# Kernel tuning notes

Hardware: AMD Instinct MI355X
Metric: run time of the kernel (lower is better)

Reference implementation:

```python
import jax, jax.numpy as jnp
import numpy as np

SIGMA = 1.0  # init kwarg sigma

def _rbf_kernel(A):
    # K[i,j] = exp(-0.5 * ||a_i - a_j||^2 / sigma^2)
    sq = jnp.sum(A * A, axis=1)                      # [n]
    d2 = sq[:, None] + sq[None, :] - 2.0 * (A @ A.T)  # [n, n]
    return jnp.exp(-0.5 * d2 / (SIGMA ** 2))

def _double_center(K):
    # C K C with C = I - 11^T/n, done in O(n^2) via mean subtraction
    row = K.mean(axis=1, keepdims=True)
    col = K.mean(axis=0, keepdims=True)
    tot = K.mean()
    return K - row - col + tot

def setup_inputs() -> dict:
    key = jax.random.key(0)
    kx, ky = jax.random.split(key)
    X = jax.random.normal(kx, (4096, 512), dtype=jnp.float32)
    Y = jax.random.normal(ky, (4096, 512), dtype=jnp.float32)
    return {"X": X, "Y": Y}

def reference(X, Y):
    n = X.shape[0]
    KXc = _double_center(_rbf_kernel(X))
    KYc = _double_center(_rbf_kernel(Y))
    # trace(KX C KY C) = sum(center(KX) * center(KY)) since K symmetric, C idempotent
    hsic = jnp.sum(KXc * KYc) / ((n - 1) ** 2)
    return hsic
```

## Files before the change

kernel.cpp:

```cpp
#include <hip/hip_runtime.h>
#include <hip/hip_bf16.h>

namespace {

constexpr int N = 4096;
constexpr int D = 512;
constexpr int BM = 64;
constexpr int BK = 64;
constexpr int KITERS = D / BK;
constexpr int NB = N / BM;
constexpr int NBLK = NB * (NB + 1) / 2;
constexpr int TILEB = BM * BK;
constexpr int PANELB = BM * D;

constexpr size_t OFF_XB  = 0;
constexpr size_t OFF_YB  = (size_t)N * D;
constexpr size_t OFF_SQX = OFF_YB + (size_t)N * D;
constexpr size_t OFF_SQY = OFF_SQX + (size_t)N * 4;
constexpr size_t OFF_SX  = OFF_SQY + (size_t)N * 4;
constexpr size_t OFF_SY  = OFF_SX + (size_t)N * 4;
constexpr size_t OFF_T1  = OFF_SY + (size_t)N * 4;
constexpr size_t WS_NEED = OFF_T1 + 4;

constexpr float D2_SKIP = 240.f;

typedef __attribute__((ext_vector_type(4))) float floatx4;
typedef __attribute__((ext_vector_type(2))) long longx2;

__device__ inline unsigned short bf16bits(float f) {
  return __builtin_bit_cast(unsigned short, __float2bfloat16(f));
}

__global__ void prep_kernel(const float* __restrict__ X, const float* __restrict__ Y,
                            unsigned char* __restrict__ Xf8, unsigned char* __restrict__ Yf8,
                            float* __restrict__ sqX, float* __restrict__ sqY,
                            float* __restrict__ sX, float* __restrict__ sY,
                            float* __restrict__ T1) {
  const int wave = threadIdx.x >> 6, lane = threadIdx.x & 63;
  const int row = blockIdx.x * 4 + wave;
  const int m = blockIdx.y;
  const float* __restrict__ src = m ? Y : X;
  unsigned char* __restrict__ dst = m ? Yf8 : Xf8;
  float* __restrict__ dsq = m ? sqY : sqX;

  if (threadIdx.x < 4) {
    float* z = m ? sY : sX;
    z[blockIdx.x * 4 + threadIdx.x] = 0.f;
  }
  if (blockIdx.x == 0 && m == 0 && threadIdx.x == 0) *T1 = 0.f;

  const float4* s4 = (const float4*)(src + (size_t)row * D);
  float4 v0 = s4[lane * 2];
  float4 v1 = s4[lane * 2 + 1];
  float acc = v0.x * v0.x + v0.y * v0.y + v0.z * v0.z + v0.w * v0.w
            + v1.x * v1.x + v1.y * v1.y + v1.z * v1.z + v1.w * v1.w;

  unsigned int w0 = 0, w1 = 0;
  w0 = __builtin_amdgcn_cvt_pk_fp8_f32(v0.x, v0.y, w0, false);
  w0 = __builtin_amdgcn_cvt_pk_fp8_f32(v0.z, v0.w, w0, true);
  w1 = __builtin_amdgcn_cvt_pk_fp8_f32(v1.x, v1.y, w1, false);
  w1 = __builtin_amdgcn_cvt_pk_fp8_f32(v1.z, v1.w, w1, true);
  const unsigned long long pk =
      (unsigned long long)w0 | ((unsigned long long)w1 << 32);

  const int p    = row >> 6;
  const int nib  = (row >> 4) & 3;
  const int cl   = row & 15;
  const int ks   = lane >> 3;
  const int pass = (lane >> 2) & 1;
  const int quad = lane & 3;
  const size_t off = (size_t)p * PANELB + (size_t)ks * TILEB +
                     nib * 1024 + quad * 256 + cl * 16 + pass * 8;
  *(unsigned long long*)(dst + off) = pk;

#pragma unroll
  for (int mm = 32; mm >= 1; mm >>= 1) acc += __shfl_xor(acc, mm, 64);
  if (lane == 0) dsq[row] = acc;
}

__launch_bounds__(256, 4)
__global__ void hsic_main(const unsigned char* __restrict__ Xf8,
                          const unsigned char* __restrict__ Yf8,
                          const float* __restrict__ sqX, const float* __restrict__ sqY,
                          float* __restrict__ sX, float* __restrict__ sY,
                          float* __restrict__ T1) {
  const int b = blockIdx.x;
  int idx = (b & 7) * (NBLK / 8) + (b >> 3);

  const float nf = (float)NB + 0.5f;
  int bI = (int)(nf - sqrtf(nf * nf - 2.0f * (float)idx));
  if (bI < 0) bI = 0;
  if (bI >= NB) bI = NB - 1;
  while (bI * NB - bI * (bI - 1) / 2 > idx) --bI;
  while ((bI + 1) * NB - (bI + 1) * bI / 2 <= idx) ++bI;
  const int bJ = bI + (idx - (bI * NB - bI * (bI - 1) / 2));
  const bool offdiag = (bI != bJ);

  const int tid = threadIdx.x;
  const int lane = tid & 63, wave = tid >> 6;
  const int wm = wave >> 1, wn = wave & 1;
  const int quad = lane >> 4, cl = lane & 15;
  const int lane16 = lane << 4;

  const unsigned char* gAx = Xf8 + (size_t)bI * PANELB + wm * 2048 + lane16;
  const unsigned char* gBx = Xf8 + (size_t)bJ * PANELB + wn * 2048 + lane16;
  const unsigned char* gAy = Yf8 + (size_t)bI * PANELB + wm * 2048 + lane16;
  const unsigned char* gBy = Yf8 + (size_t)bJ * PANELB + wn * 2048 + lane16;

  floatx4 acc[2][2];
#pragma unroll
  for (int i = 0; i < 2; ++i)
#pragma unroll
    for (int j = 0; j < 2; ++j) acc[i][j] = (floatx4){0.f, 0.f, 0.f, 0.f};

  const int Ib = bI * BM + wm * 32;
  const int Jb = bJ * BM + wn * 32;

  unsigned int kxp[2][2][2];
  unsigned int fmask = 0;
  float t1l = 0.f;

#pragma unroll
  for (int ks = 0; ks < KITERS; ++ks) {
    longx2 af[2], bf[2];
#pragma unroll
    for (int mi = 0; mi < 2; ++mi)
      af[mi] = *(const longx2*)(gAx + (size_t)ks * TILEB + mi * 1024);
#pragma unroll
    for (int ni = 0; ni < 2; ++ni)
      bf[ni] = *(const longx2*)(gBx + (size_t)ks * TILEB + ni * 1024);
#pragma unroll
    for (int mi = 0; mi < 2; ++mi)
#pragma unroll
      for (int ni = 0; ni < 2; ++ni) {
        acc[mi][ni] = __builtin_amdgcn_mfma_f32_16x16x32_fp8_fp8(af[mi][0], bf[ni][0], acc[mi][ni], 0, 0, 0);
        acc[mi][ni] = __builtin_amdgcn_mfma_f32_16x16x32_fp8_fp8(af[mi][1], bf[ni][1], acc[mi][ni], 0, 0, 0);
      }
  }

  {
    float rx[2][4];
    float cx[2];
#pragma unroll
    for (int mi = 0; mi < 2; ++mi)
#pragma unroll
      for (int r = 0; r < 4; ++r) rx[mi][r] = 0.f;
#pragma unroll
    for (int ni = 0; ni < 2; ++ni) cx[ni] = 0.f;

#pragma unroll
    for (int mi = 0; mi < 2; ++mi) {
      const int ig0 = Ib + mi * 16 + quad * 4;
      float sxi[4];
#pragma unroll
      for (int r = 0; r < 4; ++r) sxi[r] = sqX[ig0 + r];
#pragma unroll
      for (int ni = 0; ni < 2; ++ni) {
        const int jg = Jb + ni * 16 + cl;
        const float sxj = sqX[jg];
        float d2x[4];
        bool lflag = false;
#pragma unroll
        for (int r = 0; r < 4; ++r) {
          const int ig = ig0 + r;
          d2x[r] = sxi[r] + sxj - 2.f * acc[mi][ni][r];
          lflag |= (d2x[r] < D2_SKIP) | (ig == jg);
        }
        float kxv[4] = {0.f, 0.f, 0.f, 0.f};
        if (__any(lflag)) {
          fmask |= (1u << (mi * 2 + ni));
#pragma unroll
          for (int r = 0; r < 4; ++r) {
            const int ig = ig0 + r;
            kxv[r] = (ig == jg) ? 1.f : __expf(-0.5f * d2x[r]);
            rx[mi][r] += kxv[r];
            cx[ni] += kxv[r];
          }
        }
        kxp[mi][ni][0] = (unsigned)bf16bits(kxv[0]) | ((unsigned)bf16bits(kxv[1]) << 16);
        kxp[mi][ni][1] = (unsigned)bf16bits(kxv[2]) | ((unsigned)bf16bits(kxv[3]) << 16);
        acc[mi][ni] = (floatx4){0.f, 0.f, 0.f, 0.f};
      }
    }

    if (fmask != 0) {
#pragma unroll
      for (int mi = 0; mi < 2; ++mi)
#pragma unroll
        for (int r = 0; r < 4; ++r) {
          float vx = rx[mi][r];
#pragma unroll
          for (int mm = 1; mm < 16; mm <<= 1) vx += __shfl_xor(vx, mm, 16);
          rx[mi][r] = vx;
        }
      if (cl == 0) {
#pragma unroll
        for (int mi = 0; mi < 2; ++mi)
#pragma unroll
          for (int r = 0; r < 4; ++r)
            atomicAdd(&sX[Ib + mi * 16 + quad * 4 + r], rx[mi][r]);
      }
      if (offdiag) {
#pragma unroll
        for (int ni = 0; ni < 2; ++ni) {
          float vx = cx[ni];
          vx += __shfl_xor(vx, 16, 64);
          vx += __shfl_xor(vx, 32, 64);
          if (quad == 0) atomicAdd(&sX[Jb + ni * 16 + cl], vx);
        }
      }
    }
  }

#pragma unroll
  for (int ks = 0; ks < KITERS; ++ks) {
    longx2 af[2], bf[2];
#pragma unroll
    for (int mi = 0; mi < 2; ++mi)
      af[mi] = *(const longx2*)(gAy + (size_t)ks * TILEB + mi * 1024);
#pragma unroll
    for (int ni = 0; ni < 2; ++ni)
      bf[ni] = *(const longx2*)(gBy + (size_t)ks * TILEB + ni * 1024);
#pragma unroll
    for (int mi = 0; mi < 2; ++mi)
#pragma unroll
      for (int ni = 0; ni < 2; ++ni) {
        acc[mi][ni] = __builtin_amdgcn_mfma_f32_16x16x32_fp8_fp8(af[mi][0], bf[ni][0], acc[mi][ni], 0, 0, 0);
        acc[mi][ni] = __builtin_amdgcn_mfma_f32_16x16x32_fp8_fp8(af[mi][1], bf[ni][1], acc[mi][ni], 0, 0, 0);
      }
  }

  {
    float ry[2][4];
    float cy[2];
    bool anyy = false;
#pragma unroll
    for (int mi = 0; mi < 2; ++mi)
#pragma unroll
      for (int r = 0; r < 4; ++r) ry[mi][r] = 0.f;
#pragma unroll
    for (int ni = 0; ni < 2; ++ni) cy[ni] = 0.f;

#pragma unroll
    for (int mi = 0; mi < 2; ++mi) {
      const int ig0 = Ib + mi * 16 + quad * 4;
      float syi[4];
#pragma unroll
      for (int r = 0; r < 4; ++r) syi[r] = sqY[ig0 + r];
#pragma unroll
      for (int ni = 0; ni < 2; ++ni) {
        const int jg = Jb + ni * 16 + cl;
        const float syj = sqY[jg];
        float d2y[4];
        bool lflag = false;
#pragma unroll
        for (int r = 0; r < 4; ++r) {
          const int ig = ig0 + r;
          d2y[r] = syi[r] + syj - 2.f * acc[mi][ni][r];
          lflag |= (d2y[r] < D2_SKIP) | (ig == jg);
        }
        const bool xb = (fmask >> (mi * 2 + ni)) & 1u;
        if (__any(lflag) || xb) {
          anyy = true;
          float kyv[4];
#pragma unroll
          for (int r = 0; r < 4; ++r) {
            const int ig = ig0 + r;
            kyv[r] = (ig == jg) ? 1.f : __expf(-0.5f * d2y[r]);
            ry[mi][r] += kyv[r];
            cy[ni] += kyv[r];
          }
          if (xb) {
            const float kx0 = __builtin_bit_cast(float, (kxp[mi][ni][0] & 0xFFFFu) << 16);
            const float kx1 = __builtin_bit_cast(float, kxp[mi][ni][0] & 0xFFFF0000u);
            const float kx2 = __builtin_bit_cast(float, (kxp[mi][ni][1] & 0xFFFFu) << 16);
            const float kx3 = __builtin_bit_cast(float, kxp[mi][ni][1] & 0xFFFF0000u);
            t1l += kx0 * kyv[0] + kx1 * kyv[1] + kx2 * kyv[2] + kx3 * kyv[3];
          }
        }
      }
    }

    if (anyy) {
#pragma unroll
      for (int mi = 0; mi < 2; ++mi)
#pragma unroll
        for (int r = 0; r < 4; ++r) {
          float vy = ry[mi][r];
#pragma unroll
          for (int mm = 1; mm < 16; mm <<= 1) vy += __shfl_xor(vy, mm, 16);
          ry[mi][r] = vy;
        }
      if (cl == 0) {
#pragma unroll
        for (int mi = 0; mi < 2; ++mi)
#pragma unroll
          for (int r = 0; r < 4; ++r)
            atomicAdd(&sY[Ib + mi * 16 + quad * 4 + r], ry[mi][r]);
      }
      if (offdiag) {
#pragma unroll
        for (int ni = 0; ni < 2; ++ni) {
          float vy = cy[ni];
          vy += __shfl_xor(vy, 16, 64);
          vy += __shfl_xor(vy, 32, 64);
          if (quad == 0) atomicAdd(&sY[Jb + ni * 16 + cl], vy);
        }
      }
    }
  }

  if (fmask != 0) {
    t1l *= offdiag ? 2.f : 1.f;
#pragma unroll
    for (int mm = 1; mm < 64; mm <<= 1) t1l += __shfl_xor(t1l, mm, 64);
  }
  __shared__ float tred[4];
  if (lane == 0) tred[wave] = t1l;
  __syncthreads();
  if (tid == 0) {
    const float t = tred[0] + tred[1] + tred[2] + tred[3];
    if (t != 0.f) atomicAdd(T1, t);
  }
}

__global__ void final_kernel(const float* __restrict__ sX, const float* __restrict__ sY,
                             const float* __restrict__ T1, float* __restrict__ out) {
  const int tid = threadIdx.x;
  float dp = 0.f, sa = 0.f, sb = 0.f;
  for (int i = tid; i < N; i += 256) {
    float a = sX[i], b = sY[i];
    dp += a * b; sa += a; sb += b;
  }
#pragma unroll
  for (int mm = 1; mm < 64; mm <<= 1) {
    dp += __shfl_xor(dp, mm, 64);
    sa += __shfl_xor(sa, mm, 64);
    sb += __shfl_xor(sb, mm, 64);
  }
  __shared__ float r0[4], r1[4], r2[4];
  if ((tid & 63) == 0) { int w = tid >> 6; r0[w] = dp; r1[w] = sa; r2[w] = sb; }
  __syncthreads();
  if (tid == 0) {
    dp = r0[0] + r0[1] + r0[2] + r0[3];
    sa = r1[0] + r1[1] + r1[2] + r1[3];
    sb = r2[0] + r2[1] + r2[2] + r2[3];
    const float n = (float)N;
    const float total = T1[0] - (2.f / n) * dp + (sa * sb) / (n * n);
    out[0] = total / ((n - 1.f) * (n - 1.f));
  }
}

}

extern "C" void kernel_launch(void* const* d_in, const int* in_sizes, int n_in,
                              void* d_out, int out_size, void* d_ws, size_t ws_size,
                              hipStream_t stream) {
  const float* X = (const float*)d_in[0];
  const float* Y = (const float*)d_in[1];
  char* ws = (char*)d_ws;
  if (ws_size < WS_NEED) return;

  unsigned char* Xf8 = (unsigned char*)(ws + OFF_XB);
  unsigned char* Yf8 = (unsigned char*)(ws + OFF_YB);
  float* sqX = (float*)(ws + OFF_SQX);
  float* sqY = (float*)(ws + OFF_SQY);
  float* sX  = (float*)(ws + OFF_SX);
  float* sY  = (float*)(ws + OFF_SY);
  float* T1  = (float*)(ws + OFF_T1);
  float* out = (float*)d_out;

  prep_kernel<<<dim3(N / 4, 2), 256, 0, stream>>>(X, Y, Xf8, Yf8, sqX, sqY, sX, sY, T1);
  hsic_main<<<NBLK, 256, 0, stream>>>(Xf8, Yf8, sqX, sqY, sX, sY, T1);
  final_kernel<<<1, 256, 0, stream>>>(sX, sY, T1, out);
}
```

Before: 92.06 us.

## Use one wave per 64x64 tile and fold final reduction into last block

Each 64x64 output tile is now handled by a single 64-thread wave holding a 4x4 grid of MFMA accumulators, in place of four waves each holding 2x2. The per-block shared-memory reduction and barrier go away. The separate final kernel is replaced by a global completion counter: the last block to finish computes the HSIC scalar, which removes one launch. The trade-off is fewer waves in flight per CU and more registers per thread, and correctness depends on the counter wrapping modulo the block count across calls.

```diff
diff --git a/kernel.cpp b/kernel.cpp
--- a/kernel.cpp
+++ b/kernel.cpp
@@ -26,6 +26,8 @@
 
 typedef __attribute__((ext_vector_type(4))) float floatx4;
 typedef __attribute__((ext_vector_type(2))) long longx2;
+
+__device__ unsigned g_done;
 
 __device__ inline unsigned short bf16bits(float f) {
   return __builtin_bit_cast(unsigned short, __float2bfloat16(f));
@@ -78,12 +80,12 @@
   if (lane == 0) dsq[row] = acc;
 }
 
-__launch_bounds__(256, 4)
+__launch_bounds__(64, 2)
 __global__ void hsic_main(const unsigned char* __restrict__ Xf8,
                           const unsigned char* __restrict__ Yf8,
                           const float* __restrict__ sqX, const float* __restrict__ sqY,
                           float* __restrict__ sX, float* __restrict__ sY,
-                          float* __restrict__ T1) {
+                          float* __restrict__ T1, float* __restrict__ out) {
   const int b = blockIdx.x;
   int idx = (b & 7) * (NBLK / 8) + (b >> 3);
 
@@ -96,66 +98,64 @@
   const int bJ = bI + (idx - (bI * NB - bI * (bI - 1) / 2));
   const bool offdiag = (bI != bJ);
 
-  const int tid = threadIdx.x;
-  const int lane = tid & 63, wave = tid >> 6;
-  const int wm = wave >> 1, wn = wave & 1;
+  const int lane = threadIdx.x & 63;
   const int quad = lane >> 4, cl = lane & 15;
   const int lane16 = lane << 4;
 
-  const unsigned char* gAx = Xf8 + (size_t)bI * PANELB + wm * 2048 + lane16;
-  const unsigned char* gBx = Xf8 + (size_t)bJ * PANELB + wn * 2048 + lane16;
-  const unsigned char* gAy = Yf8 + (size_t)bI * PANELB + wm * 2048 + lane16;
-  const unsigned char* gBy = Yf8 + (size_t)bJ * PANELB + wn * 2048 + lane16;
-
-  floatx4 acc[2][2];
-#pragma unroll
-  for (int i = 0; i < 2; ++i)
-#pragma unroll
-    for (int j = 0; j < 2; ++j) acc[i][j] = (floatx4){0.f, 0.f, 0.f, 0.f};
-
-  const int Ib = bI * BM + wm * 32;
-  const int Jb = bJ * BM + wn * 32;
-
-  unsigned int kxp[2][2][2];
+  const unsigned char* gAx = Xf8 + (size_t)bI * PANELB + lane16;
+  const unsigned char* gBx = Xf8 + (size_t)bJ * PANELB + lane16;
+  const unsigned char* gAy = Yf8 + (size_t)bI * PANELB + lane16;
+  const unsigned char* gBy = Yf8 + (size_t)bJ * PANELB + lane16;
+
+  floatx4 acc[4][4];
+#pragma unroll
+  for (int i = 0; i < 4; ++i)
+#pragma unroll
+    for (int j = 0; j < 4; ++j) acc[i][j] = (floatx4){0.f, 0.f, 0.f, 0.f};
+
+  const int Ib = bI * BM;
+  const int Jb = bJ * BM;
+
+  unsigned int kxp[4][4][2];
   unsigned int fmask = 0;
   float t1l = 0.f;
 
 #pragma unroll
   for (int ks = 0; ks < KITERS; ++ks) {
-    longx2 af[2], bf[2];
-#pragma unroll
-    for (int mi = 0; mi < 2; ++mi)
+    longx2 af[4], bf[4];
+#pragma unroll
+    for (int mi = 0; mi < 4; ++mi)
       af[mi] = *(const longx2*)(gAx + (size_t)ks * TILEB + mi * 1024);
 #pragma unroll
-    for (int ni = 0; ni < 2; ++ni)
+    for (int ni = 0; ni < 4; ++ni)
       bf[ni] = *(const longx2*)(gBx + (size_t)ks * TILEB + ni * 1024);
 #pragma unroll
-    for (int mi = 0; mi < 2; ++mi)
-#pragma unroll
-      for (int ni = 0; ni < 2; ++ni) {
+    for (int mi = 0; mi < 4; ++mi)
+#pragma unroll
+      for (int ni = 0; ni < 4; ++ni) {
         acc[mi][ni] = __builtin_amdgcn_mfma_f32_16x16x32_fp8_fp8(af[mi][0], bf[ni][0], acc[mi][ni], 0, 0, 0);
         acc[mi][ni] = __builtin_amdgcn_mfma_f32_16x16x32_fp8_fp8(af[mi][1], bf[ni][1], acc[mi][ni], 0, 0, 0);
       }
   }
 
   {
-    float rx[2][4];
-    float cx[2];
-#pragma unroll
-    for (int mi = 0; mi < 2; ++mi)
+    float rx[4][4];
+    float cx[4];
+#pragma unroll
+    for (int mi = 0; mi < 4; ++mi)
 #pragma unroll
       for (int r = 0; r < 4; ++r) rx[mi][r] = 0.f;
 #pragma unroll
-    for (int ni = 0; ni < 2; ++ni) cx[ni] = 0.f;
-
-#pragma unroll
-    for (int mi = 0; mi < 2; ++mi) {
+    for (int ni = 0; ni < 4; ++ni) cx[ni] = 0.f;
+
+#pragma unroll
+    for (int mi = 0; mi < 4; ++mi) {
       const int ig0 = Ib + mi * 16 + quad * 4;
       float sxi[4];
 #pragma unroll
       for (int r = 0; r < 4; ++r) sxi[r] = sqX[ig0 + r];
 #pragma unroll
-      for (int ni = 0; ni < 2; ++ni) {
+      for (int ni = 0; ni < 4; ++ni) {
         const int jg = Jb + ni * 16 + cl;
         const float sxj = sqX[jg];
         float d2x[4];
@@ -168,7 +168,7 @@
         }
         float kxv[4] = {0.f, 0.f, 0.f, 0.f};
         if (__any(lflag)) {
-          fmask |= (1u << (mi * 2 + ni));
+          fmask |= (1u << (mi * 4 + ni));
 #pragma unroll
           for (int r = 0; r < 4; ++r) {
             const int ig = ig0 + r;
@@ -185,7 +185,7 @@
 
     if (fmask != 0) {
 #pragma unroll
-      for (int mi = 0; mi < 2; ++mi)
+      for (int mi = 0; mi < 4; ++mi)
 #pragma unroll
         for (int r = 0; r < 4; ++r) {
           float vx = rx[mi][r];
@@ -195,14 +195,14 @@
         }
       if (cl == 0) {
 #pragma unroll
-        for (int mi = 0; mi < 2; ++mi)
+        for (int mi = 0; mi < 4; ++mi)
 #pragma unroll
           for (int r = 0; r < 4; ++r)
             atomicAdd(&sX[Ib + mi * 16 + quad * 4 + r], rx[mi][r]);
       }
       if (offdiag) {
 #pragma unroll
-        for (int ni = 0; ni < 2; ++ni) {
+        for (int ni = 0; ni < 4; ++ni) {
           float vx = cx[ni];
           vx += __shfl_xor(vx, 16, 64);
           vx += __shfl_xor(vx, 32, 64);
@@ -214,41 +214,41 @@
 
 #pragma unroll
   for (int ks = 0; ks < KITERS; ++ks) {
-    longx2 af[2], bf[2];
-#pragma unroll
-    for (int mi = 0; mi < 2; ++mi)
+    longx2 af[4], bf[4];
+#pragma unroll
+    for (int mi = 0; mi < 4; ++mi)
       af[mi] = *(const longx2*)(gAy + (size_t)ks * TILEB + mi * 1024);
 #pragma unroll
-    for (int ni = 0; ni < 2; ++ni)
+    for (int ni = 0; ni < 4; ++ni)
       bf[ni] = *(const longx2*)(gBy + (size_t)ks * TILEB + ni * 1024);
 #pragma unroll
-    for (int mi = 0; mi < 2; ++mi)
-#pragma unroll
-      for (int ni = 0; ni < 2; ++ni) {
+    for (int mi = 0; mi < 4; ++mi)
+#pragma unroll
+      for (int ni = 0; ni < 4; ++ni) {
         acc[mi][ni] = __builtin_amdgcn_mfma_f32_16x16x32_fp8_fp8(af[mi][0], bf[ni][0], acc[mi][ni], 0, 0, 0);
         acc[mi][ni] = __builtin_amdgcn_mfma_f32_16x16x32_fp8_fp8(af[mi][1], bf[ni][1], acc[mi][ni], 0, 0, 0);
       }
   }
 
   {
-    float ry[2][4];
-    float cy[2];
+    float ry[4][4];
+    float cy[4];
     bool anyy = false;
 #pragma unroll
-    for (int mi = 0; mi < 2; ++mi)
+    for (int mi = 0; mi < 4; ++mi)
 #pragma unroll
       for (int r = 0; r < 4; ++r) ry[mi][r] = 0.f;
 #pragma unroll
-    for (int ni = 0; ni < 2; ++ni) cy[ni] = 0.f;
-
-#pragma unroll
-    for (int mi = 0; mi < 2; ++mi) {
+    for (int ni = 0; ni < 4; ++ni) cy[ni] = 0.f;
+
+#pragma unroll
+    for (int mi = 0; mi < 4; ++mi) {
       const int ig0 = Ib + mi * 16 + quad * 4;
       float syi[4];
 #pragma unroll
       for (int r = 0; r < 4; ++r) syi[r] = sqY[ig0 + r];
 #pragma unroll
-      for (int ni = 0; ni < 2; ++ni) {
+      for (int ni = 0; ni < 4; ++ni) {
         const int jg = Jb + ni * 16 + cl;
         const float syj = sqY[jg];
         float d2y[4];
@@ -259,7 +259,7 @@
           d2y[r] = syi[r] + syj - 2.f * acc[mi][ni][r];
           lflag |= (d2y[r] < D2_SKIP) | (ig == jg);
         }
-        const bool xb = (fmask >> (mi * 2 + ni)) & 1u;
+        const bool xb = (fmask >> (mi * 4 + ni)) & 1u;
         if (__any(lflag) || xb) {
           anyy = true;
           float kyv[4];
@@ -283,7 +283,7 @@
 
     if (anyy) {
 #pragma unroll
-      for (int mi = 0; mi < 2; ++mi)
+      for (int mi = 0; mi < 4; ++mi)
 #pragma unroll
         for (int r = 0; r < 4; ++r) {
           float vy = ry[mi][r];
@@ -293,14 +293,14 @@
         }
       if (cl == 0) {
 #pragma unroll
-        for (int mi = 0; mi < 2; ++mi)
+        for (int mi = 0; mi < 4; ++mi)
 #pragma unroll
           for (int r = 0; r < 4; ++r)
             atomicAdd(&sY[Ib + mi * 16 + quad * 4 + r], ry[mi][r]);
       }
       if (offdiag) {
 #pragma unroll
-        for (int ni = 0; ni < 2; ++ni) {
+        for (int ni = 0; ni < 4; ++ni) {
           float vy = cy[ni];
           vy += __shfl_xor(vy, 16, 64);
           vy += __shfl_xor(vy, 32, 64);
@@ -314,40 +314,35 @@
     t1l *= offdiag ? 2.f : 1.f;
 #pragma unroll
     for (int mm = 1; mm < 64; mm <<= 1) t1l += __shfl_xor(t1l, mm, 64);
-  }
-  __shared__ float tred[4];
-  if (lane == 0) tred[wave] = t1l;
-  __syncthreads();
-  if (tid == 0) {
-    const float t = tred[0] + tred[1] + tred[2] + tred[3];
-    if (t != 0.f) atomicAdd(T1, t);
-  }
-}
-
-__global__ void final_kernel(const float* __restrict__ sX, const float* __restrict__ sY,
-                             const float* __restrict__ T1, float* __restrict__ out) {
-  const int tid = threadIdx.x;
-  float dp = 0.f, sa = 0.f, sb = 0.f;
-  for (int i = tid; i < N; i += 256) {
-    float a = sX[i], b = sY[i];
-    dp += a * b; sa += a; sb += b;
-  }
-#pragma unroll
-  for (int mm = 1; mm < 64; mm <<= 1) {
-    dp += __shfl_xor(dp, mm, 64);
-    sa += __shfl_xor(sa, mm, 64);
-    sb += __shfl_xor(sb, mm, 64);
-  }
-  __shared__ float r0[4], r1[4], r2[4];
-  if ((tid & 63) == 0) { int w = tid >> 6; r0[w] = dp; r1[w] = sa; r2[w] = sb; }
-  __syncthreads();
-  if (tid == 0) {
-    dp = r0[0] + r0[1] + r0[2] + r0[3];
-    sa = r1[0] + r1[1] + r1[2] + r1[3];
-    sb = r2[0] + r2[1] + r2[2] + r2[3];
-    const float n = (float)N;
-    const float total = T1[0] - (2.f / n) * dp + (sa * sb) / (n * n);
-    out[0] = total / ((n - 1.f) * (n - 1.f));
+    if (lane == 0 && t1l != 0.f) atomicAdd(T1, t1l);
+  }
+
+  int am_last = 0;
+  if (lane == 0) {
+    unsigned old = __hip_atomic_fetch_add(&g_done, 1u, __ATOMIC_ACQ_REL,
+                                          __HIP_MEMORY_SCOPE_AGENT);
+    am_last = ((old + 1u) % (unsigned)NBLK) == 0u;
+  }
+  am_last = __shfl(am_last, 0, 64);
+  if (am_last) {
+    float dp = 0.f, sa = 0.f, sb = 0.f;
+    for (int i = lane; i < N; i += 64) {
+      float a = __hip_atomic_load(&sX[i], __ATOMIC_RELAXED, __HIP_MEMORY_SCOPE_AGENT);
+      float bv = __hip_atomic_load(&sY[i], __ATOMIC_RELAXED, __HIP_MEMORY_SCOPE_AGENT);
+      dp += a * bv; sa += a; sb += bv;
+    }
+#pragma unroll
+    for (int mm = 1; mm < 64; mm <<= 1) {
+      dp += __shfl_xor(dp, mm, 64);
+      sa += __shfl_xor(sa, mm, 64);
+      sb += __shfl_xor(sb, mm, 64);
+    }
+    if (lane == 0) {
+      const float t1 = __hip_atomic_load(T1, __ATOMIC_RELAXED, __HIP_MEMORY_SCOPE_AGENT);
+      const float n = (float)N;
+      const float total = t1 - (2.f / n) * dp + (sa * sb) / (n * n);
+      out[0] = total / ((n - 1.f) * (n - 1.f));
+    }
   }
 }
 
@@ -371,6 +366,5 @@
   float* out = (float*)d_out;
 
   prep_kernel<<<dim3(N / 4, 2), 256, 0, stream>>>(X, Y, Xf8, Yf8, sqX, sqY, sX, sY, T1);
-  hsic_main<<<NBLK, 256, 0, stream>>>(Xf8, Yf8, sqX, sqY, sX, sY, T1);
-  final_kernel<<<1, 256, 0, stream>>>(sX, sY, T1, out);
-}
+  hsic_main<<<NBLK, 64, 0, stream>>>(Xf8, Yf8, sqX, sqY, sX, sY, T1, out);
+}
```

After: 147.4 us. +60.1%, slower.

## Fuse final reduction into main kernel via last-wave atomic counter; spill KX to LDS

Applied to the files above, without the earlier changes.

Removes the separate final_kernel launch by having each wave increment a global done-counter; the wave that completes the launch reads the row sums and T1 and writes the result. The packed KX bf16 values move from registers into shared memory, and launch bounds are raised to 8 blocks per CU, trading register pressure for LDS so occupancy can rise. Block and wave indices are made scalar via readfirstlane, and the block-level T1 reduction becomes a per-wave atomic. The last-wave scheme depends on a persistent counter taken modulo the total wave count and on atomic visibility, which adds ordering risk.

```diff
diff --git a/kernel.cpp b/kernel.cpp
--- a/kernel.cpp
+++ b/kernel.cpp
@@ -12,6 +12,7 @@
 constexpr int NBLK = NB * (NB + 1) / 2;
 constexpr int TILEB = BM * BK;
 constexpr int PANELB = BM * D;
+constexpr unsigned WAVES_PER_LAUNCH = (unsigned)NBLK * 4u;
 
 constexpr size_t OFF_XB  = 0;
 constexpr size_t OFF_YB  = (size_t)N * D;
@@ -26,6 +27,8 @@
 
 typedef __attribute__((ext_vector_type(4))) float floatx4;
 typedef __attribute__((ext_vector_type(2))) long longx2;
+
+__device__ unsigned g_done;
 
 __device__ inline unsigned short bf16bits(float f) {
   return __builtin_bit_cast(unsigned short, __float2bfloat16(f));
@@ -78,14 +81,21 @@
   if (lane == 0) dsq[row] = acc;
 }
 
-__launch_bounds__(256, 4)
+__launch_bounds__(256, 8)
 __global__ void hsic_main(const unsigned char* __restrict__ Xf8,
                           const unsigned char* __restrict__ Yf8,
                           const float* __restrict__ sqX, const float* __restrict__ sqY,
                           float* __restrict__ sX, float* __restrict__ sY,
-                          float* __restrict__ T1) {
+                          float* __restrict__ T1, float* __restrict__ out) {
+  __shared__ unsigned long long kxs[4][256];
+
+  const int tid = threadIdx.x;
+  const int lane = tid & 63;
+  const int wv = __builtin_amdgcn_readfirstlane(tid >> 6);
+  const int wm = wv >> 1, wn = wv & 1;
+
   const int b = blockIdx.x;
-  int idx = (b & 7) * (NBLK / 8) + (b >> 3);
+  int idx = __builtin_amdgcn_readfirstlane((b & 7) * (NBLK / 8) + (b >> 3));
 
   const float nf = (float)NB + 0.5f;
   int bI = (int)(nf - sqrtf(nf * nf - 2.0f * (float)idx));
@@ -93,19 +103,18 @@
   if (bI >= NB) bI = NB - 1;
   while (bI * NB - bI * (bI - 1) / 2 > idx) --bI;
   while ((bI + 1) * NB - (bI + 1) * bI / 2 <= idx) ++bI;
-  const int bJ = bI + (idx - (bI * NB - bI * (bI - 1) / 2));
+  bI = __builtin_amdgcn_readfirstlane(bI);
+  const int bJ = __builtin_amdgcn_readfirstlane(
+      bI + (idx - (bI * NB - bI * (bI - 1) / 2)));
   const bool offdiag = (bI != bJ);
 
-  const int tid = threadIdx.x;
-  const int lane = tid & 63, wave = tid >> 6;
-  const int wm = wave >> 1, wn = wave & 1;
   const int quad = lane >> 4, cl = lane & 15;
   const int lane16 = lane << 4;
 
-  const unsigned char* gAx = Xf8 + (size_t)bI * PANELB + wm * 2048 + lane16;
-  const unsigned char* gBx = Xf8 + (size_t)bJ * PANELB + wn * 2048 + lane16;
-  const unsigned char* gAy = Yf8 + (size_t)bI * PANELB + wm * 2048 + lane16;
-  const unsigned char* gBy = Yf8 + (size_t)bJ * PANELB + wn * 2048 + lane16;
+  const unsigned char* gAx = Xf8 + (size_t)bI * PANELB + wm * 2048;
+  const unsigned char* gBx = Xf8 + (size_t)bJ * PANELB + wn * 2048;
+  const unsigned char* gAy = Yf8 + (size_t)bI * PANELB + wm * 2048;
+  const unsigned char* gBy = Yf8 + (size_t)bJ * PANELB + wn * 2048;
 
   floatx4 acc[2][2];
 #pragma unroll
@@ -116,7 +125,6 @@
   const int Ib = bI * BM + wm * 32;
   const int Jb = bJ * BM + wn * 32;
 
-  unsigned int kxp[2][2][2];
   unsigned int fmask = 0;
   float t1l = 0.f;
 
@@ -125,10 +133,10 @@
     longx2 af[2], bf[2];
 #pragma unroll
     for (int mi = 0; mi < 2; ++mi)
-      af[mi] = *(const longx2*)(gAx + (size_t)ks * TILEB + mi * 1024);
+      af[mi] = *(const longx2*)(gAx + (size_t)ks * TILEB + mi * 1024 + lane16);
 #pragma unroll
     for (int ni = 0; ni < 2; ++ni)
-      bf[ni] = *(const longx2*)(gBx + (size_t)ks * TILEB + ni * 1024);
+      bf[ni] = *(const longx2*)(gBx + (size_t)ks * TILEB + ni * 1024 + lane16);
 #pragma unroll
     for (int mi = 0; mi < 2; ++mi)
 #pragma unroll
@@ -177,8 +185,10 @@
             cx[ni] += kxv[r];
           }
         }
-        kxp[mi][ni][0] = (unsigned)bf16bits(kxv[0]) | ((unsigned)bf16bits(kxv[1]) << 16);
-        kxp[mi][ni][1] = (unsigned)bf16bits(kxv[2]) | ((unsigned)bf16bits(kxv[3]) << 16);
+        const unsigned p0 = (unsigned)bf16bits(kxv[0]) | ((unsigned)bf16bits(kxv[1]) << 16);
+        const unsigned p1 = (unsigned)bf16bits(kxv[2]) | ((unsigned)bf16bits(kxv[3]) << 16);
+        kxs[wv][(mi * 2 + ni) * 64 + lane] =
+            (unsigned long long)p0 | ((unsigned long long)p1 << 32);
         acc[mi][ni] = (floatx4){0.f, 0.f, 0.f, 0.f};
       }
     }
@@ -217,10 +227,10 @@
     longx2 af[2], bf[2];
 #pragma unroll
     for (int mi = 0; mi < 2; ++mi)
-      af[mi] = *(const longx2*)(gAy + (size_t)ks * TILEB + mi * 1024);
+      af[mi] = *(const longx2*)(gAy + (size_t)ks * TILEB + mi * 1024 + lane16);
 #pragma unroll
     for (int ni = 0; ni < 2; ++ni)
-      bf[ni] = *(const longx2*)(gBy + (size_t)ks * TILEB + ni * 1024);
+      bf[ni] = *(const longx2*)(gBy + (size_t)ks * TILEB + ni * 1024 + lane16);
 #pragma unroll
     for (int mi = 0; mi < 2; ++mi)
 #pragma unroll
@@ -271,10 +281,13 @@
             cy[ni] += kyv[r];
           }
           if (xb) {
-            const float kx0 = __builtin_bit_cast(float, (kxp[mi][ni][0] & 0xFFFFu) << 16);
-            const float kx1 = __builtin_bit_cast(float, kxp[mi][ni][0] & 0xFFFF0000u);
-            const float kx2 = __builtin_bit_cast(float, (kxp[mi][ni][1] & 0xFFFFu) << 16);
-            const float kx3 = __builtin_bit_cast(float, kxp[mi][ni][1] & 0xFFFF0000u);
+            const unsigned long long pk = kxs[wv][(mi * 2 + ni) * 64 + lane];
+            const unsigned p0 = (unsigned)pk;
+            const unsigned p1 = (unsigned)(pk >> 32);
+            const float kx0 = __builtin_bit_cast(float, (p0 & 0xFFFFu) << 16);
+            const float kx1 = __builtin_bit_cast(float, p0 & 0xFFFF0000u);
+            const float kx2 = __builtin_bit_cast(float, (p1 & 0xFFFFu) << 16);
+            const float kx3 = __builtin_bit_cast(float, p1 & 0xFFFF0000u);
             t1l += kx0 * kyv[0] + kx1 * kyv[1] + kx2 * kyv[2] + kx3 * kyv[3];
           }
         }
@@ -314,40 +327,35 @@
     t1l *= offdiag ? 2.f : 1.f;
 #pragma unroll
     for (int mm = 1; mm < 64; mm <<= 1) t1l += __shfl_xor(t1l, mm, 64);
-  }
-  __shared__ float tred[4];
-  if (lane == 0) tred[wave] = t1l;
-  __syncthreads();
-  if (tid == 0) {
-    const float t = tred[0] + tred[1] + tred[2] + tred[3];
-    if (t != 0.f) atomicAdd(T1, t);
-  }
-}
-
-__global__ void final_kernel(const float* __restrict__ sX, const float* __restrict__ sY,
-                             const float* __restrict__ T1, float* __restrict__ out) {
-  const int tid = threadIdx.x;
-  float dp = 0.f, sa = 0.f, sb = 0.f;
-  for (int i = tid; i < N; i += 256) {
-    float a = sX[i], b = sY[i];
-    dp += a * b; sa += a; sb += b;
-  }
-#pragma unroll
-  for (int mm = 1; mm < 64; mm <<= 1) {
-    dp += __shfl_xor(dp, mm, 64);
-    sa += __shfl_xor(sa, mm, 64);
-    sb += __shfl_xor(sb, mm, 64);
-  }
-  __shared__ float r0[4], r1[4], r2[4];
-  if ((tid & 63) == 0) { int w = tid >> 6; r0[w] = dp; r1[w] = sa; r2[w] = sb; }
-  __syncthreads();
-  if (tid == 0) {
-    dp = r0[0] + r0[1] + r0[2] + r0[3];
-    sa = r1[0] + r1[1] + r1[2] + r1[3];
-    sb = r2[0] + r2[1] + r2[2] + r2[3];
-    const float n = (float)N;
-    const float total = T1[0] - (2.f / n) * dp + (sa * sb) / (n * n);
-    out[0] = total / ((n - 1.f) * (n - 1.f));
+    if (lane == 0 && t1l != 0.f) atomicAdd(T1, t1l);
+  }
+
+  int am_last = 0;
+  if (lane == 0) {
+    unsigned old = __hip_atomic_fetch_add(&g_done, 1u, __ATOMIC_ACQ_REL,
+                                          __HIP_MEMORY_SCOPE_AGENT);
+    am_last = ((old + 1u) % WAVES_PER_LAUNCH) == 0u;
+  }
+  am_last = __shfl(am_last, 0, 64);
+  if (am_last) {
+    float dp = 0.f, sa = 0.f, sb = 0.f;
+    for (int i = lane; i < N; i += 64) {
+      float a = __hip_atomic_load(&sX[i], __ATOMIC_RELAXED, __HIP_MEMORY_SCOPE_AGENT);
+      float bv = __hip_atomic_load(&sY[i], __ATOMIC_RELAXED, __HIP_MEMORY_SCOPE_AGENT);
+      dp += a * bv; sa += a; sb += bv;
+    }
+#pragma unroll
+    for (int mm = 1; mm < 64; mm <<= 1) {
+      dp += __shfl_xor(dp, mm, 64);
+      sa += __shfl_xor(sa, mm, 64);
+      sb += __shfl_xor(sb, mm, 64);
+    }
+    if (lane == 0) {
+      const float t1 = __hip_atomic_load(T1, __ATOMIC_RELAXED, __HIP_MEMORY_SCOPE_AGENT);
+      const float n = (float)N;
+      const float total = t1 - (2.f / n) * dp + (sa * sb) / (n * n);
+      out[0] = total / ((n - 1.f) * (n - 1.f));
+    }
   }
 }
 
@@ -371,6 +379,5 @@
   float* out = (float*)d_out;
 
   prep_kernel<<<dim3(N / 4, 2), 256, 0, stream>>>(X, Y, Xf8, Yf8, sqX, sqY, sX, sY, T1);
-  hsic_main<<<NBLK, 256, 0, stream>>>(Xf8, Yf8, sqX, sqY, sX, sY, T1);
-  final_kernel<<<1, 256, 0, stream>>>(sX, sY, T1, out);
-}
+  hsic_main<<<NBLK, 256, 0, stream>>>(Xf8, Yf8, sqX, sqY, sX, sY, T1, out);
+}
```

New measurement: 299.4 us. 3.25x slower.

## Software-pipeline fp8 GEMM loads with inline asm double buffering across X/Y phases

Applied to the files above, without the earlier changes.

Replaces the plain unrolled K loops with hand-issued global_load_dwordx4 asm and explicit s_waitcnt, double buffering operand registers so the next K-slice loads while the current MFMAs run. The prefetch also carries across the X epilogue into the first Y tile, hiding that phase's load latency. It also removes the LDS/__syncthreads block reduction of T1 in favour of per-wave atomics and vectorises the final reduction loads. This adds register pressure and relies on exact vmcnt accounting, which could break if the compiler inserts other memory ops.

```diff
diff --git a/kernel.cpp b/kernel.cpp
--- a/kernel.cpp
+++ b/kernel.cpp
@@ -78,6 +78,39 @@
   if (lane == 0) dsq[row] = acc;
 }
 
+#define ISSUE4(A0, A1, B0, B1, PA, PB)                                       \
+  asm volatile("global_load_dwordx4 %0, %4, off\n\t"                         \
+               "global_load_dwordx4 %1, %4, off offset:1024\n\t"             \
+               "global_load_dwordx4 %2, %5, off\n\t"                         \
+               "global_load_dwordx4 %3, %5, off offset:1024"                 \
+               : "=&v"(A0), "=&v"(A1), "=&v"(B0), "=&v"(B1)                  \
+               : "v"(PA), "v"(PB)                                            \
+               : "memory")
+
+#define WAIT4(A0, A1, B0, B1, CNT)                                           \
+  asm volatile("s_waitcnt vmcnt(" CNT ")"                                    \
+               : "+v"(A0), "+v"(A1), "+v"(B0), "+v"(B1)                      \
+               :                                                             \
+               : "memory");                                                  \
+  __builtin_amdgcn_sched_barrier(0)
+
+#define MFMA_SET(A0, A1, B0, B1)                                                                  \
+  do {                                                                                            \
+    acc[0][0] = __builtin_amdgcn_mfma_f32_16x16x32_fp8_fp8((A0)[0], (B0)[0], acc[0][0], 0, 0, 0); \
+    acc[0][0] = __builtin_amdgcn_mfma_f32_16x16x32_fp8_fp8((A0)[1], (B0)[1], acc[0][0], 0, 0, 0); \
+    acc[0][1] = __builtin_amdgcn_mfma_f32_16x16x32_fp8_fp8((A0)[0], (B1)[0], acc[0][1], 0, 0, 0); \
+    acc[0][1] = __builtin_amdgcn_mfma_f32_16x16x32_fp8_fp8((A0)[1], (B1)[1], acc[0][1], 0, 0, 0); \
+    acc[1][0] = __builtin_amdgcn_mfma_f32_16x16x32_fp8_fp8((A1)[0], (B0)[0], acc[1][0], 0, 0, 0); \
+    acc[1][0] = __builtin_amdgcn_mfma_f32_16x16x32_fp8_fp8((A1)[1], (B0)[1], acc[1][0], 0, 0, 0); \
+    acc[1][1] = __builtin_amdgcn_mfma_f32_16x16x32_fp8_fp8((A1)[0], (B1)[0], acc[1][1], 0, 0, 0); \
+    acc[1][1] = __builtin_amdgcn_mfma_f32_16x16x32_fp8_fp8((A1)[1], (B1)[1], acc[1][1], 0, 0, 0); \
+  } while (0)
+
+#define STEP(IA0, IA1, IB0, IB1, UA0, UA1, UB0, UB1, PA, PB)                 \
+  ISSUE4(IA0, IA1, IB0, IB1, PA, PB);                                        \
+  WAIT4(UA0, UA1, UB0, UB1, "4");                                            \
+  MFMA_SET(UA0, UA1, UB0, UB1)
+
 __launch_bounds__(256, 4)
 __global__ void hsic_main(const unsigned char* __restrict__ Xf8,
                           const unsigned char* __restrict__ Yf8,
@@ -102,10 +135,10 @@
   const int quad = lane >> 4, cl = lane & 15;
   const int lane16 = lane << 4;
 
-  const unsigned char* gAx = Xf8 + (size_t)bI * PANELB + wm * 2048 + lane16;
-  const unsigned char* gBx = Xf8 + (size_t)bJ * PANELB + wn * 2048 + lane16;
-  const unsigned char* gAy = Yf8 + (size_t)bI * PANELB + wm * 2048 + lane16;
-  const unsigned char* gBy = Yf8 + (size_t)bJ * PANELB + wn * 2048 + lane16;
+  const unsigned char* pAx = Xf8 + (size_t)bI * PANELB + wm * 2048 + lane16;
+  const unsigned char* pBx = Xf8 + (size_t)bJ * PANELB + wn * 2048 + lane16;
+  const unsigned char* pAy = Yf8 + (size_t)bI * PANELB + wm * 2048 + lane16;
+  const unsigned char* pBy = Yf8 + (size_t)bJ * PANELB + wn * 2048 + lane16;
 
   floatx4 acc[2][2];
 #pragma unroll
@@ -120,23 +153,17 @@
   unsigned int fmask = 0;
   float t1l = 0.f;
 
-#pragma unroll
-  for (int ks = 0; ks < KITERS; ++ks) {
-    longx2 af[2], bf[2];
-#pragma unroll
-    for (int mi = 0; mi < 2; ++mi)
-      af[mi] = *(const longx2*)(gAx + (size_t)ks * TILEB + mi * 1024);
-#pragma unroll
-    for (int ni = 0; ni < 2; ++ni)
-      bf[ni] = *(const longx2*)(gBx + (size_t)ks * TILEB + ni * 1024);
-#pragma unroll
-    for (int mi = 0; mi < 2; ++mi)
-#pragma unroll
-      for (int ni = 0; ni < 2; ++ni) {
-        acc[mi][ni] = __builtin_amdgcn_mfma_f32_16x16x32_fp8_fp8(af[mi][0], bf[ni][0], acc[mi][ni], 0, 0, 0);
-        acc[mi][ni] = __builtin_amdgcn_mfma_f32_16x16x32_fp8_fp8(af[mi][1], bf[ni][1], acc[mi][ni], 0, 0, 0);
-      }
-  }
+  longx2 aP0, aP1, bP0, bP1, aQ0, aQ1, bQ0, bQ1;
+
+  ISSUE4(aP0, aP1, bP0, bP1, pAx + 0 * TILEB, pBx + 0 * TILEB);
+  STEP(aQ0, aQ1, bQ0, bQ1, aP0, aP1, bP0, bP1, pAx + 1 * TILEB, pBx + 1 * TILEB);
+  STEP(aP0, aP1, bP0, bP1, aQ0, aQ1, bQ0, bQ1, pAx + 2 * TILEB, pBx + 2 * TILEB);
+  STEP(aQ0, aQ1, bQ0, bQ1, aP0, aP1, bP0, bP1, pAx + 3 * TILEB, pBx + 3 * TILEB);
+  STEP(aP0, aP1, bP0, bP1, aQ0, aQ1, bQ0, bQ1, pAx + 4 * TILEB, pBx + 4 * TILEB);
+  STEP(aQ0, aQ1, bQ0, bQ1, aP0, aP1, bP0, bP1, pAx + 5 * TILEB, pBx + 5 * TILEB);
+  STEP(aP0, aP1, bP0, bP1, aQ0, aQ1, bQ0, bQ1, pAx + 6 * TILEB, pBx + 6 * TILEB);
+  STEP(aQ0, aQ1, bQ0, bQ1, aP0, aP1, bP0, bP1, pAx + 7 * TILEB, pBx + 7 * TILEB);
+  STEP(aP0, aP1, bP0, bP1, aQ0, aQ1, bQ0, bQ1, pAy + 0 * TILEB, pBy + 0 * TILEB);
 
   {
     float rx[2][4];
@@ -212,23 +239,15 @@
     }
   }
 
-#pragma unroll
-  for (int ks = 0; ks < KITERS; ++ks) {
-    longx2 af[2], bf[2];
-#pragma unroll
-    for (int mi = 0; mi < 2; ++mi)
-      af[mi] = *(const longx2*)(gAy + (size_t)ks * TILEB + mi * 1024);
-#pragma unroll
-    for (int ni = 0; ni < 2; ++ni)
-      bf[ni] = *(const longx2*)(gBy + (size_t)ks * TILEB + ni * 1024);
-#pragma unroll
-    for (int mi = 0; mi < 2; ++mi)
-#pragma unroll
-      for (int ni = 0; ni < 2; ++ni) {
-        acc[mi][ni] = __builtin_amdgcn_mfma_f32_16x16x32_fp8_fp8(af[mi][0], bf[ni][0], acc[mi][ni], 0, 0, 0);
-        acc[mi][ni] = __builtin_amdgcn_mfma_f32_16x16x32_fp8_fp8(af[mi][1], bf[ni][1], acc[mi][ni], 0, 0, 0);
-      }
-  }
+  STEP(aQ0, aQ1, bQ0, bQ1, aP0, aP1, bP0, bP1, pAy + 1 * TILEB, pBy + 1 * TILEB);
+  STEP(aP0, aP1, bP0, bP1, aQ0, aQ1, bQ0, bQ1, pAy + 2 * TILEB, pBy + 2 * TILEB);
+  STEP(aQ0, aQ1, bQ0, bQ1, aP0, aP1, bP0, bP1, pAy + 3 * TILEB, pBy + 3 * TILEB);
+  STEP(aP0, aP1, bP0, bP1, aQ0, aQ1, bQ0, bQ1, pAy + 4 * TILEB, pBy + 4 * TILEB);
+  STEP(aQ0, aQ1, bQ0, bQ1, aP0, aP1, bP0, bP1, pAy + 5 * TILEB, pBy + 5 * TILEB);
+  STEP(aP0, aP1, bP0, bP1, aQ0, aQ1, bQ0, bQ1, pAy + 6 * TILEB, pBy + 6 * TILEB);
+  STEP(aQ0, aQ1, bQ0, bQ1, aP0, aP1, bP0, bP1, pAy + 7 * TILEB, pBy + 7 * TILEB);
+  WAIT4(aQ0, aQ1, bQ0, bQ1, "0");
+  MFMA_SET(aQ0, aQ1, bQ0, bQ1);
 
   {
     float ry[2][4];
@@ -314,13 +333,7 @@
     t1l *= offdiag ? 2.f : 1.f;
 #pragma unroll
     for (int mm = 1; mm < 64; mm <<= 1) t1l += __shfl_xor(t1l, mm, 64);
-  }
-  __shared__ float tred[4];
-  if (lane == 0) tred[wave] = t1l;
-  __syncthreads();
-  if (tid == 0) {
-    const float t = tred[0] + tred[1] + tred[2] + tred[3];
-    if (t != 0.f) atomicAdd(T1, t);
+    if (lane == 0 && t1l != 0.f) atomicAdd(T1, t1l);
   }
 }
 
@@ -328,9 +341,12 @@
                              const float* __restrict__ T1, float* __restrict__ out) {
   const int tid = threadIdx.x;
   float dp = 0.f, sa = 0.f, sb = 0.f;
-  for (int i = tid; i < N; i += 256) {
-    float a = sX[i], b = sY[i];
-    dp += a * b; sa += a; sb += b;
+  for (int i = tid * 4; i < N; i += 1024) {
+    const float4 a4 = *(const float4*)&sX[i];
+    const float4 b4 = *(const float4*)&sY[i];
+    dp += a4.x * b4.x + a4.y * b4.y + a4.z * b4.z + a4.w * b4.w;
+    sa += a4.x + a4.y + a4.z + a4.w;
+    sb += b4.x + b4.y + b4.z + b4.w;
   }
 #pragma unroll
   for (int mm = 1; mm < 64; mm <<= 1) {
```

Measured after the change: 91.00 us, median of 2. Within noise of the previous version (-1.2%).
